# Kernel tuning notes

Measured on AMD Instinct MI355X. Metric: run time of the kernel, lower is better.

Reference implementation:

```python
import jax, jax.numpy as jnp
import numpy as np


def setup_inputs() -> dict:
    key = jax.random.key(0)
    kq, kk, kv, kb = jax.random.split(key, 4)
    B, H, S, D = 4, 16, 1024, 64
    return {
        "query": jax.random.normal(kq, (B, H, S, D), dtype=jnp.float32),
        "key": jax.random.normal(kk, (B, H, S, D), dtype=jnp.float32),
        "value": jax.random.normal(kv, (B, H, S, D), dtype=jnp.float32),
        "bias_mask": jax.random.normal(kb, (1, 1, S, S), dtype=jnp.float32),
    }


def reference(query, key, value, bias_mask):
    d_k = query.shape[-1]
    scale = 1.0 / jnp.sqrt(jnp.asarray(d_k, dtype=query.dtype))
    # scores: [B, H, Sq, Sk]
    scores = jnp.einsum("bhqd,bhkd->bhqk", query, key) * scale
    scores = scores + bias_mask
    attn_weights = jax.nn.softmax(scores, axis=-1)
    output = jnp.einsum("bhqk,bhkd->bhqd", attn_weights, value)
    return (output, attn_weights)
```

## Files before the change

kernel.cpp:

```cpp
#include <hip/hip_runtime.h>

constexpr int SEQ = 1024;
constexpr int DH  = 64;
constexpr int QR  = 32;
constexpr int KT  = 64;
constexpr int NKT = SEQ / KT;

constexpr int SK0 = 0;
constexpr int SK1 = 8192;
constexpr int SP0 = 0;
constexpr int SP1 = 4096;
constexpr int SRL = 8192;
constexpr int SV0 = 16384;
constexpr int SV1 = 24576;
constexpr int SMEM_BYTES = 32768;

typedef __bf16 bf16x8 __attribute__((ext_vector_type(8)));
typedef __bf16 bf16x4 __attribute__((ext_vector_type(4)));
typedef float  f32x4  __attribute__((ext_vector_type(4)));

__device__ __forceinline__ char* ldsa(char* s, int base, int row, int colB) {
    return s + base + row * 128 + (colB ^ ((row & 7) << 4));
}

__global__ __launch_bounds__(256, 4)
void attn_flash_kernel(const float* __restrict__ Q, const float* __restrict__ K,
                       const float* __restrict__ V, const float* __restrict__ bias,
                       float* __restrict__ out, float* __restrict__ attn)
{
    __shared__ __align__(16) char smem[SMEM_BYTES];

    const int tid = threadIdx.x;
    const int l   = tid & 63;
    const int w   = tid >> 6;
    const int qt  = w & 1;
    const int ch  = w >> 1;
    const int lm  = l & 15;
    const int lq  = l >> 4;
    const int head = blockIdx.x & 63;
    const int q0   = (blockIdx.x >> 6) * QR;
    const float scale = 0.125f;

    const float* Qh = Q + (size_t)head * SEQ * DH;
    const float* Kh = K + (size_t)head * SEQ * DH;
    const float* Vh = V + (size_t)head * SEQ * DH;
    float* outh  = out  + (size_t)head * SEQ * DH;
    float* attnh = attn + (size_t)head * SEQ * SEQ;

    const int srow = tid >> 4;
    const int sdg  = tid & 15;
    const int vkb  = tid >> 4;
    const int vdb  = tid & 15;
    const int rowg_l = qt * 16 + lq * 4;

    f32x4 kv[4];
    #pragma unroll
    for (int i = 0; i < 4; ++i)
        kv[i] = *(const f32x4*)(Kh + (size_t)(srow + 16 * i) * DH + sdg * 4);

    bf16x8 aQ[2];
    {
        const float* qrow = Qh + (size_t)(q0 + qt * 16 + lm) * DH;
        #pragma unroll
        for (int ks = 0; ks < 2; ++ks) {
            f32x4 a = *(const f32x4*)(qrow + ks * 32 + lq * 8);
            f32x4 b = *(const f32x4*)(qrow + ks * 32 + lq * 8 + 4);
            bf16x8 f;
            f[0] = (__bf16)a[0]; f[1] = (__bf16)a[1]; f[2] = (__bf16)a[2]; f[3] = (__bf16)a[3];
            f[4] = (__bf16)b[0]; f[5] = (__bf16)b[1]; f[6] = (__bf16)b[2]; f[7] = (__bf16)b[3];
            aQ[ks] = f;
        }
    }

    bf16x4 xsb[NKT][2];
    float ssum[4] = {0.f, 0.f, 0.f, 0.f};

    #pragma unroll
    for (int kt = 0; kt < NKT; ++kt) {
        const int bufK = (kt & 1) ? SK1 : SK0;
        #pragma unroll
        for (int i = 0; i < 4; ++i) {
            bf16x4 b;
            b[0] = (__bf16)kv[i][0]; b[1] = (__bf16)kv[i][1];
            b[2] = (__bf16)kv[i][2]; b[3] = (__bf16)kv[i][3];
            *(bf16x4*)ldsa(smem, bufK, srow + 16 * i, sdg * 8) = b;
        }
        __syncthreads();

        if (kt < NKT - 1) {
            #pragma unroll
            for (int i = 0; i < 4; ++i)
                kv[i] = *(const f32x4*)(Kh + (size_t)((kt + 1) * KT + srow + 16 * i) * DH + sdg * 4);
        }
        const int colg = kt * KT + ch * 32 + lm;
        float bb[4][2];
        #pragma unroll
        for (int r = 0; r < 4; ++r) {
            const float* brow = bias + (size_t)(q0 + rowg_l + r) * SEQ + colg;
            bb[r][0] = brow[0]; bb[r][1] = brow[16];
        }

        f32x4 acc[2] = {{0,0,0,0},{0,0,0,0}};
        __builtin_amdgcn_s_setprio(1);
        #pragma unroll
        for (int ks = 0; ks < 2; ++ks) {
            #pragma unroll
            for (int c = 0; c < 2; ++c) {
                bf16x8 bf = *(const bf16x8*)ldsa(smem, bufK, (ch * 2 + c) * 16 + lm, ks * 64 + lq * 16);
                acc[c] = __builtin_amdgcn_mfma_f32_16x16x32_bf16(aQ[ks], bf, acc[c], 0, 0, 0);
            }
        }
        __builtin_amdgcn_s_setprio(0);

        #pragma unroll
        for (int c = 0; c < 2; ++c) {
            #pragma unroll
            for (int r = 0; r < 4; ++r) {
                float e = __expf(acc[c][r] * scale + bb[r][c]);
                ssum[r] += e;
                xsb[kt][c][r] = (__bf16)e;
            }
        }
    }

    f32x4 vv[4];
    #pragma unroll
    for (int j = 0; j < 4; ++j)
        vv[j] = *(const f32x4*)(Vh + (size_t)(vkb * 4 + j) * DH + vdb * 4);

    #pragma unroll
    for (int r = 0; r < 4; ++r) {
        float s = ssum[r];
        #pragma unroll
        for (int off = 1; off < 16; off <<= 1)
            s += __shfl_xor(s, off);
        ssum[r] = s;
    }
    __syncthreads();
    float* sRLp = (float*)(smem + SRL);
    if (lm == 0) {
        #pragma unroll
        for (int r = 0; r < 4; ++r)
            sRLp[ch * 32 + rowg_l + r] = ssum[r];
    }
    __syncthreads();
    float linv[4];
    #pragma unroll
    for (int r = 0; r < 4; ++r)
        linv[r] = 1.0f / (sRLp[rowg_l + r] + sRLp[32 + rowg_l + r]);
    const int arow = tid >> 3;
    const int achk = tid & 7;
    const float linv_s = 1.0f / (sRLp[arow] + sRLp[32 + arow]);

    const int dtb = ch * 2;
    f32x4 oacc[2] = {{0,0,0,0},{0,0,0,0}};

    #pragma unroll
    for (int kt = 0; kt < NKT; ++kt) {
        const int bufP = (kt & 1) ? SP1 : SP0;
        const int bufV = (kt & 1) ? SV1 : SV0;

        #pragma unroll
        for (int jj = 0; jj < 4; ++jj) {
            bf16x4 b;
            b[0] = (__bf16)vv[0][jj]; b[1] = (__bf16)vv[1][jj];
            b[2] = (__bf16)vv[2][jj]; b[3] = (__bf16)vv[3][jj];
            *(bf16x4*)ldsa(smem, bufV, vdb * 4 + jj, vkb * 8) = b;
        }
        #pragma unroll
        for (int c = 0; c < 2; ++c)
            #pragma unroll
            for (int r = 0; r < 4; ++r)
                *(__bf16*)ldsa(smem, bufP, rowg_l + r, (ch * 32 + c * 16 + lm) * 2) = xsb[kt][c][r];
        __syncthreads();

        if (kt < NKT - 1) {
            #pragma unroll
            for (int j = 0; j < 4; ++j)
                vv[j] = *(const f32x4*)(Vh + (size_t)((kt + 1) * KT + vkb * 4 + j) * DH + vdb * 4);
        }

        {
            bf16x4 pa = *(const bf16x4*)ldsa(smem, bufP, arow, achk * 8);
            bf16x4 pb = *(const bf16x4*)ldsa(smem, bufP, arow, 64 + achk * 8);
            f32x4 wa, wb;
            #pragma unroll
            for (int i = 0; i < 4; ++i) { wa[i] = (float)pa[i] * linv_s; wb[i] = (float)pb[i] * linv_s; }
            float* ap = attnh + (size_t)(q0 + arow) * SEQ + kt * KT;
            __builtin_nontemporal_store(wa, (f32x4*)(ap + achk * 4));
            __builtin_nontemporal_store(wb, (f32x4*)(ap + 32 + achk * 4));
        }

        __builtin_amdgcn_s_setprio(1);
        #pragma unroll
        for (int ks = 0; ks < 2; ++ks) {
            bf16x8 af = *(const bf16x8*)ldsa(smem, bufP, qt * 16 + lm, ks * 64 + lq * 16);
            #pragma unroll
            for (int c = 0; c < 2; ++c) {
                bf16x8 bf = *(const bf16x8*)ldsa(smem, bufV, (dtb + c) * 16 + lm, ks * 64 + lq * 16);
                oacc[c] = __builtin_amdgcn_mfma_f32_16x16x32_bf16(af, bf, oacc[c], 0, 0, 0);
            }
        }
        __builtin_amdgcn_s_setprio(0);
    }

    #pragma unroll
    for (int c = 0; c < 2; ++c)
        #pragma unroll
        for (int r = 0; r < 4; ++r)
            __builtin_nontemporal_store(oacc[c][r] * linv[r],
                outh + (size_t)(q0 + rowg_l + r) * DH + (dtb + c) * 16 + lm);
}

extern "C" void kernel_launch(void* const* d_in, const int* in_sizes, int n_in,
                              void* d_out, int out_size, void* d_ws, size_t ws_size,
                              hipStream_t stream) {
    const float* Q    = (const float*)d_in[0];
    const float* K    = (const float*)d_in[1];
    const float* V    = (const float*)d_in[2];
    const float* bias = (const float*)d_in[3];
    float* out  = (float*)d_out;
    float* attn = (float*)d_out + 4 * 16 * 1024 * 64;
    dim3 grid(64 * (SEQ / QR));
    dim3 block(256);
    attn_flash_kernel<<<grid, block, 0, stream>>>(Q, K, V, bias, out, attn);
}
```

Baseline: 516.4 us.

## Double key tile to 128 columns and rework LDS layout for V/P stages

Raises the key tile from 64 to 128 so each block processes half as many tile iterations and barriers, with each wave computing four 16-column score fragments instead of two. K and V now share double-buffered LDS regions, and the V/P buffers use a 256-byte row stride with a wider XOR swizzle. The attention-weight store is remapped so each wave writes full contiguous 512-byte rows. The cost is more registers (larger prefetch arrays) and more LDS, with launch bounds lowered from 4 to 3 blocks per CU, which may reduce occupancy.

```diff
diff --git a/kernel.cpp b/kernel.cpp
--- a/kernel.cpp
+++ b/kernel.cpp
@@ -3,27 +3,28 @@
 constexpr int SEQ = 1024;
 constexpr int DH  = 64;
 constexpr int QR  = 32;
-constexpr int KT  = 64;
+constexpr int KT  = 128;
 constexpr int NKT = SEQ / KT;
 
-constexpr int SK0 = 0;
-constexpr int SK1 = 8192;
-constexpr int SP0 = 0;
-constexpr int SP1 = 4096;
-constexpr int SRL = 8192;
-constexpr int SV0 = 16384;
-constexpr int SV1 = 24576;
-constexpr int SMEM_BYTES = 32768;
+constexpr int SA0 = 0;
+constexpr int SA1 = 16384;
+constexpr int SP0 = 32768;
+constexpr int SP1 = 40960;
+constexpr int SRL = 49152;
+constexpr int SMEM_BYTES = 49408;
 
 typedef __bf16 bf16x8 __attribute__((ext_vector_type(8)));
 typedef __bf16 bf16x4 __attribute__((ext_vector_type(4)));
 typedef float  f32x4  __attribute__((ext_vector_type(4)));
 
-__device__ __forceinline__ char* ldsa(char* s, int base, int row, int colB) {
+__device__ __forceinline__ char* kadr(char* s, int base, int row, int colB) {
     return s + base + row * 128 + (colB ^ ((row & 7) << 4));
 }
-
-__global__ __launch_bounds__(256, 4)
+__device__ __forceinline__ char* vadr(char* s, int base, int row, int colB) {
+    return s + base + row * 256 + (colB ^ ((row & 15) << 4));
+}
+
+__global__ __launch_bounds__(256, 3)
 void attn_flash_kernel(const float* __restrict__ Q, const float* __restrict__ K,
                        const float* __restrict__ V, const float* __restrict__ bias,
                        float* __restrict__ out, float* __restrict__ attn)
@@ -49,13 +50,13 @@
 
     const int srow = tid >> 4;
     const int sdg  = tid & 15;
-    const int vkb  = tid >> 4;
-    const int vdb  = tid & 15;
+    const int vkb  = tid & 31;
+    const int vdb0 = tid >> 5;
     const int rowg_l = qt * 16 + lq * 4;
 
-    f32x4 kv[4];
-    #pragma unroll
-    for (int i = 0; i < 4; ++i)
+    f32x4 kv[8];
+    #pragma unroll
+    for (int i = 0; i < 8; ++i)
         kv[i] = *(const f32x4*)(Kh + (size_t)(srow + 16 * i) * DH + sdg * 4);
 
     bf16x8 aQ[2];
@@ -72,48 +73,48 @@
         }
     }
 
-    bf16x4 xsb[NKT][2];
+    bf16x4 xsb[NKT][4];
     float ssum[4] = {0.f, 0.f, 0.f, 0.f};
 
     #pragma unroll
     for (int kt = 0; kt < NKT; ++kt) {
-        const int bufK = (kt & 1) ? SK1 : SK0;
-        #pragma unroll
-        for (int i = 0; i < 4; ++i) {
+        const int bufK = (kt & 1) ? SA1 : SA0;
+        #pragma unroll
+        for (int i = 0; i < 8; ++i) {
             bf16x4 b;
             b[0] = (__bf16)kv[i][0]; b[1] = (__bf16)kv[i][1];
             b[2] = (__bf16)kv[i][2]; b[3] = (__bf16)kv[i][3];
-            *(bf16x4*)ldsa(smem, bufK, srow + 16 * i, sdg * 8) = b;
+            *(bf16x4*)kadr(smem, bufK, srow + 16 * i, sdg * 8) = b;
         }
         __syncthreads();
 
         if (kt < NKT - 1) {
             #pragma unroll
-            for (int i = 0; i < 4; ++i)
+            for (int i = 0; i < 8; ++i)
                 kv[i] = *(const f32x4*)(Kh + (size_t)((kt + 1) * KT + srow + 16 * i) * DH + sdg * 4);
         }
-        const int colg = kt * KT + ch * 32 + lm;
-        float bb[4][2];
+        const int colg = kt * KT + ch * 64 + lm;
+        float bb[4][4];
         #pragma unroll
         for (int r = 0; r < 4; ++r) {
             const float* brow = bias + (size_t)(q0 + rowg_l + r) * SEQ + colg;
-            bb[r][0] = brow[0]; bb[r][1] = brow[16];
-        }
-
-        f32x4 acc[2] = {{0,0,0,0},{0,0,0,0}};
+            bb[r][0] = brow[0]; bb[r][1] = brow[16]; bb[r][2] = brow[32]; bb[r][3] = brow[48];
+        }
+
+        f32x4 acc[4] = {{0,0,0,0},{0,0,0,0},{0,0,0,0},{0,0,0,0}};
         __builtin_amdgcn_s_setprio(1);
         #pragma unroll
         for (int ks = 0; ks < 2; ++ks) {
             #pragma unroll
-            for (int c = 0; c < 2; ++c) {
-                bf16x8 bf = *(const bf16x8*)ldsa(smem, bufK, (ch * 2 + c) * 16 + lm, ks * 64 + lq * 16);
+            for (int c = 0; c < 4; ++c) {
+                bf16x8 bf = *(const bf16x8*)kadr(smem, bufK, (ch * 4 + c) * 16 + lm, ks * 64 + lq * 16);
                 acc[c] = __builtin_amdgcn_mfma_f32_16x16x32_bf16(aQ[ks], bf, acc[c], 0, 0, 0);
             }
         }
         __builtin_amdgcn_s_setprio(0);
 
         #pragma unroll
-        for (int c = 0; c < 2; ++c) {
+        for (int c = 0; c < 4; ++c) {
             #pragma unroll
             for (int r = 0; r < 4; ++r) {
                 float e = __expf(acc[c][r] * scale + bb[r][c]);
@@ -123,11 +124,6 @@
         }
     }
 
-    f32x4 vv[4];
-    #pragma unroll
-    for (int j = 0; j < 4; ++j)
-        vv[j] = *(const f32x4*)(Vh + (size_t)(vkb * 4 + j) * DH + vdb * 4);
-
     #pragma unroll
     for (int r = 0; r < 4; ++r) {
         float s = ssum[r];
@@ -136,7 +132,13 @@
             s += __shfl_xor(s, off);
         ssum[r] = s;
     }
-    __syncthreads();
+    f32x4 vv[2][4];
+    #pragma unroll
+    for (int i = 0; i < 2; ++i)
+        #pragma unroll
+        for (int jj = 0; jj < 4; ++jj)
+            vv[i][jj] = *(const f32x4*)(Vh + (size_t)(vkb * 4 + jj) * DH + (vdb0 + 8 * i) * 4);
+
     float* sRLp = (float*)(smem + SRL);
     if (lm == 0) {
         #pragma unroll
@@ -144,60 +146,69 @@
             sRLp[ch * 32 + rowg_l + r] = ssum[r];
     }
     __syncthreads();
-    float linv[4];
+
+    float linv[4], linv_st[4];
     #pragma unroll
     for (int r = 0; r < 4; ++r)
         linv[r] = 1.0f / (sRLp[rowg_l + r] + sRLp[32 + rowg_l + r]);
-    const int arow = tid >> 3;
-    const int achk = tid & 7;
-    const float linv_s = 1.0f / (sRLp[arow] + sRLp[32 + arow]);
+    #pragma unroll
+    for (int j = 0; j < 4; ++j) {
+        int row = (w << 3) + 2 * j + (l >> 5);
+        linv_st[j] = 1.0f / (sRLp[row] + sRLp[32 + row]);
+    }
 
     const int dtb = ch * 2;
     f32x4 oacc[2] = {{0,0,0,0},{0,0,0,0}};
 
     #pragma unroll
     for (int kt = 0; kt < NKT; ++kt) {
+        const int bufV = (kt & 1) ? SA1 : SA0;
         const int bufP = (kt & 1) ? SP1 : SP0;
-        const int bufV = (kt & 1) ? SV1 : SV0;
-
-        #pragma unroll
-        for (int jj = 0; jj < 4; ++jj) {
-            bf16x4 b;
-            b[0] = (__bf16)vv[0][jj]; b[1] = (__bf16)vv[1][jj];
-            b[2] = (__bf16)vv[2][jj]; b[3] = (__bf16)vv[3][jj];
-            *(bf16x4*)ldsa(smem, bufV, vdb * 4 + jj, vkb * 8) = b;
-        }
-        #pragma unroll
-        for (int c = 0; c < 2; ++c)
+
+        #pragma unroll
+        for (int i = 0; i < 2; ++i) {
+            int d0 = (vdb0 + 8 * i) * 4;
+            #pragma unroll
+            for (int jj = 0; jj < 4; ++jj) {
+                bf16x4 b;
+                b[0] = (__bf16)vv[i][0][jj]; b[1] = (__bf16)vv[i][1][jj];
+                b[2] = (__bf16)vv[i][2][jj]; b[3] = (__bf16)vv[i][3][jj];
+                *(bf16x4*)vadr(smem, bufV, d0 + jj, vkb * 8) = b;
+            }
+        }
+        #pragma unroll
+        for (int c = 0; c < 4; ++c)
             #pragma unroll
             for (int r = 0; r < 4; ++r)
-                *(__bf16*)ldsa(smem, bufP, rowg_l + r, (ch * 32 + c * 16 + lm) * 2) = xsb[kt][c][r];
+                *(__bf16*)vadr(smem, bufP, rowg_l + r, ch * 128 + 32 * c + 2 * lm) = xsb[kt][c][r];
         __syncthreads();
 
         if (kt < NKT - 1) {
             #pragma unroll
-            for (int j = 0; j < 4; ++j)
-                vv[j] = *(const f32x4*)(Vh + (size_t)((kt + 1) * KT + vkb * 4 + j) * DH + vdb * 4);
-        }
-
-        {
-            bf16x4 pa = *(const bf16x4*)ldsa(smem, bufP, arow, achk * 8);
-            bf16x4 pb = *(const bf16x4*)ldsa(smem, bufP, arow, 64 + achk * 8);
-            f32x4 wa, wb;
-            #pragma unroll
-            for (int i = 0; i < 4; ++i) { wa[i] = (float)pa[i] * linv_s; wb[i] = (float)pb[i] * linv_s; }
-            float* ap = attnh + (size_t)(q0 + arow) * SEQ + kt * KT;
-            __builtin_nontemporal_store(wa, (f32x4*)(ap + achk * 4));
-            __builtin_nontemporal_store(wb, (f32x4*)(ap + 32 + achk * 4));
+            for (int i = 0; i < 2; ++i)
+                #pragma unroll
+                for (int jj = 0; jj < 4; ++jj)
+                    vv[i][jj] = *(const f32x4*)(Vh + (size_t)((kt + 1) * KT + vkb * 4 + jj) * DH + (vdb0 + 8 * i) * 4);
+        }
+
+        #pragma unroll
+        for (int j = 0; j < 4; ++j) {
+            const int row = (w << 3) + 2 * j + (l >> 5);
+            bf16x4 pv = *(const bf16x4*)vadr(smem, bufP, row, (l & 31) * 8);
+            f32x4 wv;
+            #pragma unroll
+            for (int i = 0; i < 4; ++i) wv[i] = (float)pv[i] * linv_st[j];
+            __builtin_nontemporal_store(wv,
+                (f32x4*)(attnh + (size_t)(q0 + row) * SEQ + kt * KT + (l & 31) * 4));
         }
 
         __builtin_amdgcn_s_setprio(1);
         #pragma unroll
-        for (int ks = 0; ks < 2; ++ks) {
-            bf16x8 af = *(const bf16x8*)ldsa(smem, bufP, qt * 16 + lm, ks * 64 + lq * 16);
+        for (int ks = 0; ks < 4; ++ks) {
+            bf16x8 af = *(const bf16x8*)vadr(smem, bufP, qt * 16 + lm, ks * 64 + lq * 16);
             #pragma unroll
             for (int c = 0; c < 2; ++c) {
-                bf16x8 bf = *(const bf16x8*)ldsa(smem, bufV, (dtb + c) * 16 + lm, ks * 64 + lq * 16);
+                bf16x8 bf = *(const bf16x8*)vadr(smem, bufV, (dtb + c) * 16 + lm, ks * 64 + lq * 16);
                 oacc[c] = __builtin_amdgcn_mfma_f32_16x16x32_bf16(af, bf, oacc[c], 0, 0, 0);
             }
         }
```

Result: faster. 497.7 us (-3.6%).
